# Performance work log

Measured on AMD Instinct MI355X. Metric: run time of the kernel, lower is better.

Reference implementation:

```python
import jax, jax.numpy as jnp
import numpy as np

B = 2_000_000  # number of 6x6 stiffness matrices

def setup_inputs() -> dict:
    key = jax.random.key(0)
    C = jax.random.normal(key, (B, 6, 6), dtype=jnp.float32)
    return {"C": C}

def reference(C) -> jnp.ndarray:
    # matrix_power_4: C^4 via two repeated squarings, batched over leading dim
    C2 = jnp.matmul(C, C)   # [B,6,6]
    return jnp.matmul(C2, C2)
```

## Files before the change

kernel.cpp:

```cpp
#include <hip/hip_runtime.h>


#define MPB 256
#define NB  1024

#define GLOBAL_AS __attribute__((address_space(1)))
#define LDS_AS    __attribute__((address_space(3)))

typedef float f32x4 __attribute__((ext_vector_type(4)));

__device__ __forceinline__ void pow4_regs(float a[36])
{
    float b[36];
#pragma unroll
    for (int i = 0; i < 6; ++i)
#pragma unroll
        for (int j = 0; j < 6; ++j) {
            float s = a[i * 6 + 0] * a[0 * 6 + j];
#pragma unroll
            for (int k = 1; k < 6; ++k)
                s = fmaf(a[i * 6 + k], a[k * 6 + j], s);
            b[i * 6 + j] = s;
        }
#pragma unroll
    for (int i = 0; i < 6; ++i)
#pragma unroll
        for (int j = 0; j < 6; ++j) {
            float s = b[i * 6 + 0] * b[0 * 6 + j];
#pragma unroll
            for (int k = 1; k < 6; ++k)
                s = fmaf(b[i * 6 + k], b[k * 6 + j], s);
            a[i * 6 + j] = s;
        }
}

__global__ __launch_bounds__(256, 4) void matpow4_persist(
    const float* __restrict__ C, float* __restrict__ out, int nchunk, int B)
{
    __shared__ f32x4 lds4[MPB * 9];

    const int tid = threadIdx.x;
    const int bid = blockIdx.x;

    const f32x4* __restrict__ srcAll = reinterpret_cast<const f32x4*>(C);
    f32x4* __restrict__ dstAll = reinterpret_cast<f32x4*>(out);

    for (int c = bid; c < nchunk; c += NB) {
        const f32x4* src = srcAll + (size_t)c * (MPB * 9);

#pragma unroll
        for (int k = 0; k < 9; ++k) {
            int f = k * MPB + tid;
            __builtin_amdgcn_global_load_lds(
                (const GLOBAL_AS void*)(src + f),
                (LDS_AS void*)(&lds4[f]), 16, 0,  2);
        }
        __syncthreads();

        {
            float a[36];
#pragma unroll
            for (int j = 0; j < 9; ++j) {
                f32x4 v = lds4[tid * 9 + j];
                a[4 * j + 0] = v.x;
                a[4 * j + 1] = v.y;
                a[4 * j + 2] = v.z;
                a[4 * j + 3] = v.w;
            }
            pow4_regs(a);
#pragma unroll
            for (int j = 0; j < 9; ++j) {
                f32x4 v;
                v.x = a[4 * j + 0];
                v.y = a[4 * j + 1];
                v.z = a[4 * j + 2];
                v.w = a[4 * j + 3];
                lds4[tid * 9 + j] = v;
            }
        }
        __syncthreads();

#pragma unroll
        for (int k = 0; k < 9; ++k) {
            int f = k * MPB + tid;
            f32x4 v = lds4[f];
            __builtin_nontemporal_store(v, dstAll + (size_t)c * (MPB * 9) + f);
        }

        asm volatile("s_waitcnt lgkmcnt(0)" ::: "memory");
        asm volatile("s_barrier" ::: "memory");
    }

    if (bid == NB - 1) {
        int idx = nchunk * MPB + tid;
        if (idx < B) {
            const f32x4* src = srcAll + (size_t)idx * 9;
            float a[36];
#pragma unroll
            for (int j = 0; j < 9; ++j) {
                f32x4 v = src[j];
                a[4 * j + 0] = v.x;
                a[4 * j + 1] = v.y;
                a[4 * j + 2] = v.z;
                a[4 * j + 3] = v.w;
            }
            pow4_regs(a);
            f32x4* dst = dstAll + (size_t)idx * 9;
#pragma unroll
            for (int j = 0; j < 9; ++j) {
                f32x4 v;
                v.x = a[4 * j + 0];
                v.y = a[4 * j + 1];
                v.z = a[4 * j + 2];
                v.w = a[4 * j + 3];
                dst[j] = v;
            }
        }
    }
}

extern "C" void kernel_launch(void* const* d_in, const int* in_sizes, int n_in,
                              void* d_out, int out_size, void* d_ws, size_t ws_size,
                              hipStream_t stream)
{
    const float* C = (const float*)d_in[0];
    float* out = (float*)d_out;
    int B = in_sizes[0] / 36;

    int nchunk = B / MPB;
    matpow4_persist<<<NB, MPB, 0, stream>>>(C, out, nchunk, B);
}
```

Before: 109.9 us.

## Replace persistent 256-thread blocks with one-wave blocks using waitcnt instead of barriers

```diff
diff --git a/kernel.cpp b/kernel.cpp
--- a/kernel.cpp
+++ b/kernel.cpp
@@ -1,8 +1,7 @@
 #include <hip/hip_runtime.h>
 
 
-#define MPB 256
-#define NB  1024
+#define WPB 64
 
 #define GLOBAL_AS __attribute__((address_space(1)))
 #define LDS_AS    __attribute__((address_space(3)))
@@ -34,67 +33,61 @@
         }
 }
 
-__global__ __launch_bounds__(256, 4) void matpow4_persist(
-    const float* __restrict__ C, float* __restrict__ out, int nchunk, int B)
+__global__ __launch_bounds__(WPB, 4) void matpow4_wave(
+    const float* __restrict__ C, float* __restrict__ out, int nfull, int B)
 {
-    __shared__ f32x4 lds4[MPB * 9];
+    __shared__ f32x4 lds4[WPB * 9];
 
-    const int tid = threadIdx.x;
+    const int lane = threadIdx.x;
     const int bid = blockIdx.x;
 
-    const f32x4* __restrict__ srcAll = reinterpret_cast<const f32x4*>(C);
-    f32x4* __restrict__ dstAll = reinterpret_cast<f32x4*>(out);
-
-    for (int c = bid; c < nchunk; c += NB) {
-        const f32x4* src = srcAll + (size_t)c * (MPB * 9);
+    if (bid < nfull) {
+        const f32x4* __restrict__ src =
+            reinterpret_cast<const f32x4*>(C) + (size_t)bid * (WPB * 9);
+        f32x4* __restrict__ dst =
+            reinterpret_cast<f32x4*>(out) + (size_t)bid * (WPB * 9);
 
 #pragma unroll
         for (int k = 0; k < 9; ++k) {
-            int f = k * MPB + tid;
+            int f = k * WPB + lane;
             __builtin_amdgcn_global_load_lds(
                 (const GLOBAL_AS void*)(src + f),
-                (LDS_AS void*)(&lds4[f]), 16, 0,  2);
+                (LDS_AS void*)(&lds4[f]), 16, 0, 0);
         }
-        __syncthreads();
+        asm volatile("s_waitcnt vmcnt(0)" ::: "memory");
+        __builtin_amdgcn_sched_barrier(0);
 
-        {
-            float a[36];
+        float a[36];
 #pragma unroll
-            for (int j = 0; j < 9; ++j) {
-                f32x4 v = lds4[tid * 9 + j];
-                a[4 * j + 0] = v.x;
-                a[4 * j + 1] = v.y;
-                a[4 * j + 2] = v.z;
-                a[4 * j + 3] = v.w;
-            }
-            pow4_regs(a);
+        for (int j = 0; j < 9; ++j) {
+            f32x4 v = lds4[lane * 9 + j];
+            a[4 * j + 0] = v.x;
+            a[4 * j + 1] = v.y;
+            a[4 * j + 2] = v.z;
+            a[4 * j + 3] = v.w;
+        }
+        pow4_regs(a);
 #pragma unroll
-            for (int j = 0; j < 9; ++j) {
-                f32x4 v;
-                v.x = a[4 * j + 0];
-                v.y = a[4 * j + 1];
-                v.z = a[4 * j + 2];
-                v.w = a[4 * j + 3];
-                lds4[tid * 9 + j] = v;
-            }
+        for (int j = 0; j < 9; ++j) {
+            f32x4 v;
+            v.x = a[4 * j + 0];
+            v.y = a[4 * j + 1];
+            v.z = a[4 * j + 2];
+            v.w = a[4 * j + 3];
+            lds4[lane * 9 + j] = v;
         }
-        __syncthreads();
+        asm volatile("s_waitcnt lgkmcnt(0)" ::: "memory");
+        __builtin_amdgcn_sched_barrier(0);
 
 #pragma unroll
         for (int k = 0; k < 9; ++k) {
-            int f = k * MPB + tid;
-            f32x4 v = lds4[f];
-            __builtin_nontemporal_store(v, dstAll + (size_t)c * (MPB * 9) + f);
+            int f = k * WPB + lane;
+            dst[f] = lds4[f];
         }
-
-        asm volatile("s_waitcnt lgkmcnt(0)" ::: "memory");
-        asm volatile("s_barrier" ::: "memory");
-    }
-
-    if (bid == NB - 1) {
-        int idx = nchunk * MPB + tid;
+    } else {
+        int idx = nfull * WPB + lane;
         if (idx < B) {
-            const f32x4* src = srcAll + (size_t)idx * 9;
+            const f32x4* src = reinterpret_cast<const f32x4*>(C) + (size_t)idx * 9;
             float a[36];
 #pragma unroll
             for (int j = 0; j < 9; ++j) {
@@ -105,7 +98,7 @@
                 a[4 * j + 3] = v.w;
             }
             pow4_regs(a);
-            f32x4* dst = dstAll + (size_t)idx * 9;
+            f32x4* dst = reinterpret_cast<f32x4*>(out) + (size_t)idx * 9;
 #pragma unroll
             for (int j = 0; j < 9; ++j) {
                 f32x4 v;
@@ -127,6 +120,7 @@
     float* out = (float*)d_out;
     int B = in_sizes[0] / 36;
 
-    int nchunk = B / MPB;
-    matpow4_persist<<<NB, MPB, 0, stream>>>(C, out, nchunk, B);
+    int nfull = B / WPB;
+    int grid = nfull + ((B % WPB) ? 1 : 0);
+    matpow4_wave<<<grid, WPB, 0, stream>>>(C, out, nfull, B);
 }
```

Result: no change. 111.1 us (+1.1%).
